# Optimization experiments

Measured on AMD Instinct MI355X. Metric: run time of the kernel, lower is better.

## Reference

```python
import jax, jax.numpy as jnp
import numpy as np

N, E, B = 200000, 6400000, 128
IN_LOCAL, IN_GLOBAL, HIDDEN, NUM_CLASSES = 16, 8, 32, 2


def setup_inputs() -> dict:
    key = jax.random.key(0)
    ks = jax.random.split(key, 16)
    inp = {
        "x_local": jax.random.normal(ks[0], (N, IN_LOCAL), dtype=jnp.float32),
        "x_global": jax.random.normal(ks[1], (B, IN_GLOBAL), dtype=jnp.float32),
        "batch": jnp.sort(jax.random.randint(ks[2], (N,), 0, B, dtype=jnp.int64)),
        "edge_index": jax.random.randint(ks[3], (2, E), 0, N, dtype=jnp.int64),
        # encoder params
        "W_local": jax.random.normal(ks[4], (IN_LOCAL, HIDDEN), jnp.float32) / np.sqrt(IN_LOCAL),
        "b_local": jnp.zeros((HIDDEN,), jnp.float32),
        "W_global": jax.random.normal(ks[5], (IN_GLOBAL, HIDDEN), jnp.float32) / np.sqrt(IN_GLOBAL),
        "b_global": jnp.zeros((HIDDEN,), jnp.float32),
        "W_mix": jax.random.normal(ks[6], (3 * HIDDEN, HIDDEN), jnp.float32) / np.sqrt(3 * HIDDEN),
        "b_mix": jnp.zeros((HIDDEN,), jnp.float32),
        # GNN layer params
        "W_msg": jax.random.normal(ks[7], (HIDDEN, HIDDEN), jnp.float32) / np.sqrt(HIDDEN),
        "b_msg": jnp.zeros((HIDDEN,), jnp.float32),
        "W_self": jax.random.normal(ks[8], (HIDDEN, HIDDEN), jnp.float32) / np.sqrt(HIDDEN),
        "b_self": jnp.zeros((HIDDEN,), jnp.float32),
        # output head
        "W_out": jax.random.normal(ks[9], (HIDDEN, NUM_CLASSES), jnp.float32) / np.sqrt(HIDDEN),
        "b_out": jnp.zeros((NUM_CLASSES,), jnp.float32),
    }
    return inp


def reference(x_local, x_global, batch, edge_index,
              W_local, b_local, W_global, b_global, W_mix, b_mix,
              W_msg, b_msg, W_self, b_self, W_out, b_out):
    n = x_local.shape[0]
    # --- MixedSelectivityNodeEncoder ---
    h_local = jax.nn.relu(x_local @ W_local + b_local)            # [N,H]
    h_global_graph = jax.nn.relu(x_global @ W_global + b_global)  # [B,H]
    h_global = h_global_graph[batch]                              # gather -> [N,H]
    h_int = h_local * h_global
    h_cat = jnp.concatenate([h_local, h_global, h_int], axis=-1)  # [N,3H]
    h0 = jax.nn.relu(h_cat @ W_mix + b_mix)                       # [N,H]
    # --- GNN layer with self loops, add aggregation ---
    loops = jnp.arange(n, dtype=edge_index.dtype)
    src = jnp.concatenate([edge_index[0], loops])                 # [E+N]
    dst = jnp.concatenate([edge_index[1], loops])                 # [E+N]
    msg = jax.nn.relu(h0[src] @ W_msg + b_msg)                    # [E+N,H]
    aggr = jax.ops.segment_sum(msg, dst, num_segments=n)          # [N,H]
    h = jax.nn.relu(aggr + h0 @ W_self + b_self)                  # [N,H]
    # --- output head ---
    return h @ W_out + b_out                                      # [N,C]
```

## Files before the change

kernel.cpp:

```cpp
#include <hip/hip_runtime.h>

#define N_NODES  200000
#define N_EDGES  6400000
#define NGRAPH   128
#define H        32

#define BNODES   256
#define NBUCK    782
#define P_BLOCKS 256
#define EPB      25000
#define SORT_CAP 10240

typedef unsigned short ushort_t;

__device__ __forceinline__ ushort_t f32_to_bf16_rne(float f) {
    unsigned u = __float_as_uint(f);
    unsigned r = (u + 0x7fffu + ((u >> 16) & 1u)) >> 16;
    return (ushort_t)r;
}
__device__ __forceinline__ float bf16_to_f32(ushort_t h) {
    return __uint_as_float(((unsigned)h) << 16);
}

__global__ __launch_bounds__(256) void k_node_enc(
        const float* __restrict__ xl,
        const int*   __restrict__ batch,
        const float* __restrict__ xg,   const float* __restrict__ Wg,
        const float* __restrict__ bg,
        const float* __restrict__ Wl,   const float* __restrict__ bl,
        const float* __restrict__ Wmix, const float* __restrict__ bmix,
        const float* __restrict__ Wmsg, const float* __restrict__ bmsg,
        const float* __restrict__ Wself,const float* __restrict__ bself,
        ushort_t* __restrict__ mb, float* __restrict__ s) {
    int n0 = blockIdx.x * 256 + threadIdx.x;
    bool valid = (n0 < N_NODES);
    int n = valid ? n0 : (N_NODES - 1);

    float xv[16];
    {
        const float4* p = (const float4*)(xl + (size_t)n * 16);
        float4 a = p[0], b = p[1], c = p[2], d = p[3];
        xv[0]=a.x; xv[1]=a.y; xv[2]=a.z; xv[3]=a.w;
        xv[4]=b.x; xv[5]=b.y; xv[6]=b.z; xv[7]=b.w;
        xv[8]=c.x; xv[9]=c.y; xv[10]=c.z; xv[11]=c.w;
        xv[12]=d.x; xv[13]=d.y; xv[14]=d.z; xv[15]=d.w;
    }
    float gvv[8];
    {
        int gb = batch[n];
        const float4* q = (const float4*)(xg + (size_t)gb * 8);
        float4 a = q[0], b = q[1];
        gvv[0]=a.x; gvv[1]=a.y; gvv[2]=a.z; gvv[3]=a.w;
        gvv[4]=b.x; gvv[5]=b.y; gvv[6]=b.z; gvv[7]=b.w;
    }

    float hl[32], hg[32], hi[32];
#pragma unroll
    for (int t4 = 0; t4 < 8; ++t4) {
        float4 al = ((const float4*)bl)[t4];
        float4 ag = ((const float4*)bg)[t4];
#pragma unroll
        for (int k = 0; k < 16; ++k) {
            float4 w = ((const float4*)(Wl + k * H))[t4];
            al.x = fmaf(xv[k], w.x, al.x); al.y = fmaf(xv[k], w.y, al.y);
            al.z = fmaf(xv[k], w.z, al.z); al.w = fmaf(xv[k], w.w, al.w);
        }
#pragma unroll
        for (int k = 0; k < 8; ++k) {
            float4 w = ((const float4*)(Wg + k * H))[t4];
            ag.x = fmaf(gvv[k], w.x, ag.x); ag.y = fmaf(gvv[k], w.y, ag.y);
            ag.z = fmaf(gvv[k], w.z, ag.z); ag.w = fmaf(gvv[k], w.w, ag.w);
        }
        hl[t4*4+0] = fmaxf(al.x, 0.f); hl[t4*4+1] = fmaxf(al.y, 0.f);
        hl[t4*4+2] = fmaxf(al.z, 0.f); hl[t4*4+3] = fmaxf(al.w, 0.f);
        hg[t4*4+0] = fmaxf(ag.x, 0.f); hg[t4*4+1] = fmaxf(ag.y, 0.f);
        hg[t4*4+2] = fmaxf(ag.z, 0.f); hg[t4*4+3] = fmaxf(ag.w, 0.f);
    }
#pragma unroll
    for (int k = 0; k < 32; ++k) hi[k] = hl[k] * hg[k];

    float h0[32];
#pragma unroll
    for (int t4 = 0; t4 < 8; ++t4) {
        float4 acc = ((const float4*)bmix)[t4];
#pragma unroll
        for (int k = 0; k < 32; ++k) {
            float4 w = ((const float4*)(Wmix + k * H))[t4];
            acc.x = fmaf(hl[k], w.x, acc.x); acc.y = fmaf(hl[k], w.y, acc.y);
            acc.z = fmaf(hl[k], w.z, acc.z); acc.w = fmaf(hl[k], w.w, acc.w);
        }
#pragma unroll
        for (int k = 0; k < 32; ++k) {
            float4 w = ((const float4*)(Wmix + (32 + k) * H))[t4];
            acc.x = fmaf(hg[k], w.x, acc.x); acc.y = fmaf(hg[k], w.y, acc.y);
            acc.z = fmaf(hg[k], w.z, acc.z); acc.w = fmaf(hg[k], w.w, acc.w);
        }
#pragma unroll
        for (int k = 0; k < 32; ++k) {
            float4 w = ((const float4*)(Wmix + (64 + k) * H))[t4];
            acc.x = fmaf(hi[k], w.x, acc.x); acc.y = fmaf(hi[k], w.y, acc.y);
            acc.z = fmaf(hi[k], w.z, acc.z); acc.w = fmaf(hi[k], w.w, acc.w);
        }
        h0[t4*4+0] = fmaxf(acc.x, 0.f); h0[t4*4+1] = fmaxf(acc.y, 0.f);
        h0[t4*4+2] = fmaxf(acc.z, 0.f); h0[t4*4+3] = fmaxf(acc.w, 0.f);
    }

#pragma unroll
    for (int t4 = 0; t4 < 8; ++t4) {
        float4 am = ((const float4*)bmsg)[t4];
        float4 as = ((const float4*)bself)[t4];
#pragma unroll
        for (int k = 0; k < 32; ++k) {
            float4 wm = ((const float4*)(Wmsg + k * H))[t4];
            float4 ws = ((const float4*)(Wself + k * H))[t4];
            am.x = fmaf(h0[k], wm.x, am.x); am.y = fmaf(h0[k], wm.y, am.y);
            am.z = fmaf(h0[k], wm.z, am.z); am.w = fmaf(h0[k], wm.w, am.w);
            as.x = fmaf(h0[k], ws.x, as.x); as.y = fmaf(h0[k], ws.y, as.y);
            as.z = fmaf(h0[k], ws.z, as.z); as.w = fmaf(h0[k], ws.w, as.w);
        }
        if (valid) {
            unsigned d0 = (unsigned)f32_to_bf16_rne(fmaxf(am.x, 0.f))
                        | ((unsigned)f32_to_bf16_rne(fmaxf(am.y, 0.f)) << 16);
            unsigned d1 = (unsigned)f32_to_bf16_rne(fmaxf(am.z, 0.f))
                        | ((unsigned)f32_to_bf16_rne(fmaxf(am.w, 0.f)) << 16);
            ((unsigned*)(mb + (size_t)n * H))[t4*2+0] = d0;
            ((unsigned*)(mb + (size_t)n * H))[t4*2+1] = d1;
            ((float4*)(s + (size_t)n * H))[t4] = as;
        }
    }
}

__global__ __launch_bounds__(1024) void k_pcount(const int* __restrict__ ei,
                                                 int* __restrict__ gcnt) {
    __shared__ int cnt[NBUCK];
    int t = threadIdx.x, blk = blockIdx.x;
    for (int i = t; i < NBUCK; i += 1024) cnt[i] = 0;
    __syncthreads();
    int e1 = (blk + 1) * EPB;
    for (int e = blk * EPB + t; e < e1; e += 1024)
        atomicAdd(&cnt[ei[N_EDGES + e] >> 8], 1);
    __syncthreads();
    for (int i = t; i < NBUCK; i += 1024)
        gcnt[i * P_BLOCKS + blk] = cnt[i];
}

__global__ void k_blocksum_g(const int* __restrict__ gcnt, int* __restrict__ bsum) {
    int b = blockIdx.x, t = threadIdx.x;
    int v = gcnt[b * P_BLOCKS + t];
#pragma unroll
    for (int off = 32; off >= 1; off >>= 1)
        v += __shfl_down(v, off, 64);
    __shared__ int w4[4];
    if ((t & 63) == 0) w4[t >> 6] = v;
    __syncthreads();
    if (t == 0) bsum[b] = w4[0] + w4[1] + w4[2] + w4[3];
}

__global__ void k_scan_bsums_g(const int* __restrict__ bsum, int* __restrict__ boff) {
    __shared__ int sd[1024];
    int t = threadIdx.x;
    sd[t] = (t < NBUCK) ? bsum[t] : 0;
    __syncthreads();
#pragma unroll
    for (int off = 1; off < 1024; off <<= 1) {
        int v = (t >= off) ? sd[t - off] : 0;
        __syncthreads();
        sd[t] += v;
        __syncthreads();
    }
    if (t < NBUCK) boff[t] = (t == 0) ? 0 : sd[t - 1];
}

__global__ void k_make_cursor_g(int* __restrict__ gcnt, const int* __restrict__ boff) {
    __shared__ int sd[P_BLOCKS];
    int b = blockIdx.x, t = threadIdx.x, i = b * P_BLOCKS + t;
    int c = gcnt[i];
    sd[t] = c;
    __syncthreads();
#pragma unroll
    for (int off = 1; off < P_BLOCKS; off <<= 1) {
        int v = (t >= off) ? sd[t - off] : 0;
        __syncthreads();
        sd[t] += v;
        __syncthreads();
    }
    gcnt[i] = boff[b] + sd[t] - c;
}

__global__ __launch_bounds__(1024) void k_pscatter(const int* __restrict__ ei,
                                                   const int* __restrict__ goff,
                                                   unsigned int* __restrict__ ebuf) {
    __shared__ int cur[NBUCK];
    int t = threadIdx.x, blk = blockIdx.x;
    for (int i = t; i < NBUCK; i += 1024) cur[i] = goff[i * P_BLOCKS + blk];
    __syncthreads();
    int e1 = (blk + 1) * EPB;
    for (int e = blk * EPB + t; e < e1; e += 1024) {
        unsigned src = (unsigned)ei[e];
        int dst = ei[N_EDGES + e];
        int pos = atomicAdd(&cur[dst >> 8], 1);
        ebuf[pos] = (src << 8) | (unsigned)(dst & 255);
    }
}

__global__ __launch_bounds__(512) void k_bsort(const int* __restrict__ goff,
                                               unsigned int* __restrict__ ebuf,
                                               int* __restrict__ row_start) {
    __shared__ unsigned sorted[SORT_CAP];
    __shared__ int cnt[BNODES];
    __shared__ int off[BNODES];
    __shared__ int cur[BNODES];
    int tid = threadIdx.x, b = blockIdx.x;

    int bs = goff[b * P_BLOCKS];
    int be = (b == NBUCK - 1) ? N_EDGES : goff[(b + 1) * P_BLOCKS];

    if (tid < BNODES) cnt[tid] = 0;
    __syncthreads();

    for (int j = bs + tid; j < be; j += 512)
        atomicAdd(&cnt[ebuf[j] & 255], 1);
    __syncthreads();

    if (tid < BNODES) off[tid] = cnt[tid];
    __syncthreads();
#pragma unroll
    for (int d = 1; d < BNODES; d <<= 1) {
        int v = (tid < BNODES && tid >= d) ? off[tid - d] : 0;
        __syncthreads();
        if (tid < BNODES) off[tid] += v;
        __syncthreads();
    }
    if (tid < BNODES) cur[tid] = off[tid] - cnt[tid];
    __syncthreads();

    for (int j = bs + tid; j < be; j += 512) {
        unsigned pk = ebuf[j];
        int pos = atomicAdd(&cur[pk & 255], 1);
        sorted[pos] = pk;
    }
    __syncthreads();

    int sz = be - bs;
    for (int i = tid; i < sz; i += 512)
        ebuf[bs + i] = sorted[i] >> 8;

    if (tid < BNODES) {
        int n = b * BNODES + tid;
        if (n <= N_NODES)
            row_start[n] = bs + (off[tid] - cnt[tid]);
    }
}

__global__ __launch_bounds__(256) void k_aggr_final(
        const int* __restrict__ row_start,
        const int* __restrict__ csr,
        const ushort_t* __restrict__ mb, const float* __restrict__ s,
        const float* __restrict__ Wout, const float* __restrict__ bout,
        float* __restrict__ out) {
    int tid   = threadIdx.x;
    int local = tid >> 5;
    int t     = tid & 31;
    int n     = blockIdx.x * 8 + local;

    int start = row_start[n];
    int end   = row_start[n + 1];

    float a[8];
#pragma unroll
    for (int k = 0; k < 8; ++k) a[k] = 0.f;

    for (int j = start; j < end; j += 8) {
        int idx[8];
#pragma unroll
        for (int k = 0; k < 8; ++k)
            idx[k] = csr[min(j + k, end - 1)];
        float v[8];
#pragma unroll
        for (int k = 0; k < 8; ++k)
            v[k] = bf16_to_f32(mb[idx[k] * H + t]);
#pragma unroll
        for (int k = 0; k < 8; ++k)
            a[k] += (j + k < end) ? v[k] : 0.f;
    }
    float acc = ((a[0] + a[1]) + (a[2] + a[3])) + ((a[4] + a[5]) + (a[6] + a[7]));

    int i = n * H + t;
    float h = fmaxf(acc + bf16_to_f32(mb[i]) + s[i], 0.f);

    float p0 = h * Wout[t * 2 + 0];
    float p1 = h * Wout[t * 2 + 1];
#pragma unroll
    for (int off = 16; off >= 1; off >>= 1) {
        p0 += __shfl_down(p0, off, 32);
        p1 += __shfl_down(p1, off, 32);
    }
    if (t == 0) {
        out[n * 2 + 0] = p0 + bout[0];
        out[n * 2 + 1] = p1 + bout[1];
    }
}

extern "C" void kernel_launch(void* const* d_in, const int* in_sizes, int n_in,
                              void* d_out, int out_size, void* d_ws, size_t ws_size,
                              hipStream_t stream) {
    const float* xl    = (const float*)d_in[0];
    const float* xg    = (const float*)d_in[1];
    const int*   batch = (const int*)  d_in[2];
    const int*   ei    = (const int*)  d_in[3];
    const float* Wl    = (const float*)d_in[4];
    const float* bl    = (const float*)d_in[5];
    const float* Wg    = (const float*)d_in[6];
    const float* bg    = (const float*)d_in[7];
    const float* Wmix  = (const float*)d_in[8];
    const float* bmix  = (const float*)d_in[9];
    const float* Wmsg  = (const float*)d_in[10];
    const float* bmsg  = (const float*)d_in[11];
    const float* Wself = (const float*)d_in[12];
    const float* bself = (const float*)d_in[13];
    const float* Wout  = (const float*)d_in[14];
    const float* bout  = (const float*)d_in[15];
    float* out = (float*)d_out;

    float*    s    = (float*)d_ws;
    ushort_t* mb   = (ushort_t*)(s + (size_t)N_NODES * H);
    int*      gcnt = (int*)(mb + (size_t)N_NODES * H);
    int*      bsum = gcnt + (size_t)NBUCK * P_BLOCKS;
    int*      boff = bsum + NBUCK;
    int*      row_start = boff + NBUCK;
    unsigned int* ebuf = (unsigned int*)(row_start + N_NODES + 2);

    k_node_enc<<<(N_NODES + 255) / 256, 256, 0, stream>>>(xl, batch, xg, Wg, bg,
                                                          Wl, bl, Wmix, bmix,
                                                          Wmsg, bmsg, Wself, bself,
                                                          mb, s);

    k_pcount<<<P_BLOCKS, 1024, 0, stream>>>(ei, gcnt);
    k_blocksum_g<<<NBUCK, P_BLOCKS, 0, stream>>>(gcnt, bsum);
    k_scan_bsums_g<<<1, 1024, 0, stream>>>(bsum, boff);
    k_make_cursor_g<<<NBUCK, P_BLOCKS, 0, stream>>>(gcnt, boff);
    k_pscatter<<<P_BLOCKS, 1024, 0, stream>>>(ei, gcnt, ebuf);

    k_bsort<<<NBUCK, 512, 0, stream>>>(gcnt, ebuf, row_start);

    k_aggr_final<<<N_NODES / 8, 256, 0, stream>>>(row_start, (const int*)ebuf,
                                                  mb, s, Wout, bout, out);
}
```

Before: 381.0 us.

## Fuse bucket sort with neighbor aggregation and output head in one kernel

The per-bucket sort kernel now runs the aggregation directly from its shared-memory sorted edge list. This removes the write-back of the CSR array and row_start to global memory and the separate aggregation launch. Each 16-lane group handles 8 nodes, loading two bf16 features per lane as one 32-bit word. The risk is lower parallelism: only 782 blocks of 512 threads do the gather phase, which may expose gather latency compared with the earlier 25000-block aggregation launch.

```diff
diff --git a/kernel.cpp b/kernel.cpp
--- a/kernel.cpp
+++ b/kernel.cpp
@@ -203,9 +203,12 @@
     }
 }
 
-__global__ __launch_bounds__(512) void k_bsort(const int* __restrict__ goff,
-                                               unsigned int* __restrict__ ebuf,
-                                               int* __restrict__ row_start) {
+__global__ __launch_bounds__(512) void k_bsort_aggr(
+        const int* __restrict__ goff,
+        const unsigned int* __restrict__ ebuf,
+        const ushort_t* __restrict__ mb, const float* __restrict__ s,
+        const float* __restrict__ Wout, const float* __restrict__ bout,
+        float* __restrict__ out) {
     __shared__ unsigned sorted[SORT_CAP];
     __shared__ int cnt[BNODES];
     __shared__ int off[BNODES];
@@ -241,63 +244,53 @@
     }
     __syncthreads();
 
-    int sz = be - bs;
-    for (int i = tid; i < sz; i += 512)
-        ebuf[bs + i] = sorted[i] >> 8;
-
-    if (tid < BNODES) {
-        int n = b * BNODES + tid;
-        if (n <= N_NODES)
-            row_start[n] = bs + (off[tid] - cnt[tid]);
-    }
-}
-
-__global__ __launch_bounds__(256) void k_aggr_final(
-        const int* __restrict__ row_start,
-        const int* __restrict__ csr,
-        const ushort_t* __restrict__ mb, const float* __restrict__ s,
-        const float* __restrict__ Wout, const float* __restrict__ bout,
-        float* __restrict__ out) {
-    int tid   = threadIdx.x;
-    int local = tid >> 5;
-    int t     = tid & 31;
-    int n     = blockIdx.x * 8 + local;
-
-    int start = row_start[n];
-    int end   = row_start[n + 1];
-
-    float a[8];
-#pragma unroll
-    for (int k = 0; k < 8; ++k) a[k] = 0.f;
-
-    for (int j = start; j < end; j += 8) {
-        int idx[8];
-#pragma unroll
-        for (int k = 0; k < 8; ++k)
-            idx[k] = csr[min(j + k, end - 1)];
-        float v[8];
-#pragma unroll
-        for (int k = 0; k < 8; ++k)
-            v[k] = bf16_to_f32(mb[idx[k] * H + t]);
-#pragma unroll
-        for (int k = 0; k < 8; ++k)
-            a[k] += (j + k < end) ? v[k] : 0.f;
-    }
-    float acc = ((a[0] + a[1]) + (a[2] + a[3])) + ((a[4] + a[5]) + (a[6] + a[7]));
-
-    int i = n * H + t;
-    float h = fmaxf(acc + bf16_to_f32(mb[i]) + s[i], 0.f);
-
-    float p0 = h * Wout[t * 2 + 0];
-    float p1 = h * Wout[t * 2 + 1];
-#pragma unroll
-    for (int off = 16; off >= 1; off >>= 1) {
-        p0 += __shfl_down(p0, off, 32);
-        p1 += __shfl_down(p1, off, 32);
-    }
-    if (t == 0) {
-        out[n * 2 + 0] = p0 + bout[0];
-        out[n * 2 + 1] = p1 + bout[1];
+    const unsigned* mb32 = (const unsigned*)mb;
+    int g = tid >> 4;
+    int t = tid & 15;
+
+    for (int q = 0; q < 8; ++q) {
+        int loc = (g << 3) + q;
+        int n = b * BNODES + loc;
+        int rs = off[loc] - cnt[loc];
+        int re = off[loc];
+        float a0 = 0.f, a1 = 0.f;
+
+        for (int j = rs; j < re; j += 8) {
+            unsigned pk[8], u[8];
+#pragma unroll
+            for (int k = 0; k < 8; ++k)
+                pk[k] = sorted[min(j + k, re - 1)];
+#pragma unroll
+            for (int k = 0; k < 8; ++k)
+                u[k] = mb32[(pk[k] >> 8) * 16u + (unsigned)t];
+#pragma unroll
+            for (int k = 0; k < 8; ++k) {
+                bool ok = (j + k < re);
+                a0 += ok ? __uint_as_float(u[k] << 16)         : 0.f;
+                a1 += ok ? __uint_as_float(u[k] & 0xffff0000u) : 0.f;
+            }
+        }
+
+        if (n < N_NODES) {
+            unsigned u = mb32[(unsigned)n * 16u + (unsigned)t];
+            float2 sv = *(const float2*)(s + (size_t)n * H + 2 * t);
+            float h0 = fmaxf(a0 + __uint_as_float(u << 16)         + sv.x, 0.f);
+            float h1 = fmaxf(a1 + __uint_as_float(u & 0xffff0000u) + sv.y, 0.f);
+            float4 w = *(const float4*)(Wout + 4 * t);
+            float p0 = h0 * w.x + h1 * w.z;
+            float p1 = h0 * w.y + h1 * w.w;
+#pragma unroll
+            for (int o = 8; o >= 1; o >>= 1) {
+                p0 += __shfl_down(p0, o, 16);
+                p1 += __shfl_down(p1, o, 16);
+            }
+            if (t == 0) {
+                float2 o2;
+                o2.x = p0 + bout[0];
+                o2.y = p1 + bout[1];
+                *(float2*)(out + (size_t)n * 2) = o2;
+            }
+        }
     }
 }
 
@@ -327,8 +320,7 @@
     int*      gcnt = (int*)(mb + (size_t)N_NODES * H);
     int*      bsum = gcnt + (size_t)NBUCK * P_BLOCKS;
     int*      boff = bsum + NBUCK;
-    int*      row_start = boff + NBUCK;
-    unsigned int* ebuf = (unsigned int*)(row_start + N_NODES + 2);
+    unsigned int* ebuf = (unsigned int*)(boff + NBUCK);
 
     k_node_enc<<<(N_NODES + 255) / 256, 256, 0, stream>>>(xl, batch, xg, Wg, bg,
                                                           Wl, bl, Wmix, bmix,
@@ -341,8 +333,5 @@
     k_make_cursor_g<<<NBUCK, P_BLOCKS, 0, stream>>>(gcnt, boff);
     k_pscatter<<<P_BLOCKS, 1024, 0, stream>>>(ei, gcnt, ebuf);
 
-    k_bsort<<<NBUCK, 512, 0, stream>>>(gcnt, ebuf, row_start);
-
-    k_aggr_final<<<N_NODES / 8, 256, 0, stream>>>(row_start, (const int*)ebuf,
-                                                  mb, s, Wout, bout, out);
-}
+    k_bsort_aggr<<<NBUCK, 512, 0, stream>>>(gcnt, ebuf, mb, s, Wout, bout, out);
+}
```

Result: slower. 389.1 us (+2.1%).
